# Kernel optimization log

Hardware: AMD Instinct MI355X
Metric: run time of the kernel (lower is better)

The kernel has to match this reference:

```python
import jax, jax.numpy as jnp
import numpy as np


def setup_inputs() -> dict:
    key = jax.random.key(0)
    k1, k2, k3, k4, k5 = jax.random.split(key, 5)
    B, H, W, C = 4, 64, 64, 512
    ratio = 8
    d = C // ratio  # 64
    x = jax.random.normal(k1, (B, H, W, C), dtype=jnp.float32)
    # 1x1 conv weights (no bias) == channel-mixing matrices, he_normal-ish scale
    Wq = jax.random.normal(k2, (C, d), dtype=jnp.float32) * np.sqrt(2.0 / C)
    Wk = jax.random.normal(k3, (C, d), dtype=jnp.float32) * np.sqrt(2.0 / C)
    Wv = jax.random.normal(k4, (C, C), dtype=jnp.float32) * np.sqrt(2.0 / C)
    gamma = jax.random.normal(k5, (1,), dtype=jnp.float32)
    return {"x": x, "Wq": Wq, "Wk": Wk, "Wv": Wv, "gamma": gamma}


def reference(x, Wq, Wk, Wv, gamma):
    B, H, W, C = x.shape
    N = H * W
    # 1x1 convs (no bias) are per-pixel channel matmuls
    q = jnp.einsum('bhwc,cd->bhwd', x, Wq).reshape(B, N, -1)  # [B,N,d]
    k = jnp.einsum('bhwc,cd->bhwd', x, Wk).reshape(B, N, -1)  # [B,N,d]
    v = jnp.einsum('bhwc,cd->bhwd', x, Wv).reshape(B, N, C)   # [B,N,C]
    # energy[b,i,j] = key_i . query_j  (batch_dot(key, query^T))
    energy = jnp.einsum('bid,bjd->bij', k, q)                 # [B,N,N]
    attn = jax.nn.softmax(energy, axis=-1)
    out = jnp.einsum('bij,bjc->bic', attn, v)                 # [B,N,C]
    out = out.reshape(B, H, W, C)
    return gamma * out
```

## Files before the change

kernel.cpp:

```cpp
#include <hip/hip_runtime.h>
#include <hip/hip_bf16.h>

typedef unsigned short u16;
typedef unsigned int   u32;
typedef __attribute__((ext_vector_type(8))) short short8;
typedef __attribute__((ext_vector_type(4))) float f32x4;
typedef __attribute__((ext_vector_type(4))) u16   u16x4;

#define MFMA16(a,b,c) __builtin_amdgcn_mfma_f32_16x16x32_bf16((a),(b),(c),0,0,0)

#define BATCH 4
#define NPIX  4096
#define CCH   512
#define DDIM  64
#define MFIX  64.0f

static __device__ __forceinline__ u16 f2bf(float f){
  __hip_bfloat16 h = __float2bfloat16(f);
  return __builtin_bit_cast(u16, h);
}
static __device__ __forceinline__ float bf2f(u16 u){
  __hip_bfloat16 h = __builtin_bit_cast(__hip_bfloat16, u);
  return __bfloat162float(h);
}

__global__ __launch_bounds__(256) void k_wconv(const f32x4* __restrict__ wv,
                                               u16x4* __restrict__ wvb){
  const int i = blockIdx.x*256 + threadIdx.x;
  #pragma unroll
  for (int it=0; it<4; ++it){
    int idx = i + it*16384;
    f32x4 v = wv[idx];
    u16x4 o;
    o[0]=f2bf(v[0]); o[1]=f2bf(v[1]); o[2]=f2bf(v[2]); o[3]=f2bf(v[3]);
    wvb[idx] = o;
  }
}

__global__ __launch_bounds__(256) void k_qkproj(const float* __restrict__ x,
                                                const float* __restrict__ Wq,
                                                const float* __restrict__ Wk,
                                                u16* __restrict__ qhi, u16* __restrict__ qlo,
                                                u16* __restrict__ khi, u16* __restrict__ klo,
                                                u16* __restrict__ xhi){
  __shared__ float xs[32][512];
  const int pix0 = blockIdx.x * 32;
  {
    const f32x4* xg = (const f32x4*)(x + (size_t)pix0*CCH);
    f32x4* xsv = (f32x4*)(&xs[0][0]);
    #pragma unroll
    for (int it=0; it<16; ++it) xsv[threadIdx.x + it*256] = xg[threadIdx.x + it*256];
  }
  __syncthreads();
  #pragma unroll
  for (int e=0; e<16; ++e){
    int idx4 = e*256 + threadIdx.x;
    int f = idx4*4;
    int row = f >> 9, col = f & 511;
    f32x4 v = *(const f32x4*)(&xs[row][col]);
    u16x4 o;
    o[0]=f2bf(v[0]); o[1]=f2bf(v[1]); o[2]=f2bf(v[2]); o[3]=f2bf(v[3]);
    *(u16x4*)(&xhi[(size_t)(pix0+row)*CCH + col]) = o;
  }
  const int col = threadIdx.x & 127;
  const int grp = threadIdx.x >> 7;
  const float* W = (col < 64) ? Wq : Wk;
  const int wc = col & 63;
  float acc[16];
  #pragma unroll
  for (int p=0;p<16;++p) acc[p] = 0.f;
  #pragma unroll 2
  for (int c=0;c<512;c+=4){
    float w0 = W[(c+0)*64 + wc];
    float w1 = W[(c+1)*64 + wc];
    float w2 = W[(c+2)*64 + wc];
    float w3 = W[(c+3)*64 + wc];
    #pragma unroll
    for (int p=0;p<16;++p){
      f32x4 xv = *(const f32x4*)(&xs[grp*16+p][c]);
      acc[p] += xv[0]*w0 + xv[1]*w1 + xv[2]*w2 + xv[3]*w3;
    }
  }
  #pragma unroll
  for (int p=0;p<16;++p){
    int pix = pix0 + grp*16 + p;
    float v = acc[p];
    u16 hi = f2bf(v);
    u16 lo = f2bf(v - bf2f(hi));
    if (col < 64){ qhi[pix*64+wc] = hi; qlo[pix*64+wc] = lo; }
    else         { khi[pix*64+wc] = hi; klo[pix*64+wc] = lo; }
  }
}

__global__ __launch_bounds__(256) void k_vproj(const u16* __restrict__ xhi,
                                               const u16* __restrict__ wvb,
                                               u16* __restrict__ vJB){
  __shared__ u16 As[64][72];
  __shared__ u16 Bs[64][266];
  const int pix0 = blockIdx.x * 64;
  const int c0   = blockIdx.y * 256;
  const int tid = threadIdx.x;
  const int w = tid >> 6, l = tid & 63;
  const int lg = l >> 4, ll = l & 15;
  f32x4 acc[4][4];
  #pragma unroll
  for (int mf=0;mf<4;++mf)
    #pragma unroll
    for (int nf=0;nf<4;++nf){ f32x4 z = {0.f,0.f,0.f,0.f}; acc[mf][nf] = z; }

  for (int ks=0; ks<8; ++ks){
    __syncthreads();
    #pragma unroll
    for (int it=0; it<2; ++it){
      int ch = tid + it*256; int r = ch>>3, c8 = ch&7;
      *(uint4*)(&As[r][c8*8]) = *(const uint4*)(&xhi[(size_t)(pix0+r)*CCH + ks*64 + c8*8]);
    }
    #pragma unroll
    for (int it=0; it<8; ++it){
      int ch = tid + it*256; int r = ch>>5, c32 = ch&31;
      uint4 d = *(const uint4*)(&wvb[(size_t)(ks*64+r)*CCH + c0 + c32*8]);
      u32* dst = (u32*)(&Bs[r][c32*8]);
      dst[0]=d.x; dst[1]=d.y; dst[2]=d.z; dst[3]=d.w;
    }
    __syncthreads();
    #pragma unroll
    for (int kc=0;kc<2;++kc){
      short8 a[4];
      #pragma unroll
      for (int mf=0;mf<4;++mf) a[mf] = *(const short8*)(&As[mf*16 + ll][kc*32 + lg*8]);
      #pragma unroll
      for (int nf=0;nf<4;++nf){
        short8 bb;
        int cc = w*64 + nf*16 + ll;
        #pragma unroll
        for (int e=0;e<8;++e) bb[e] = (short)Bs[kc*32 + lg*8 + e][cc];
        #pragma unroll
        for (int mf=0;mf<4;++mf) acc[mf][nf] = MFMA16(a[mf], bb, acc[mf][nf]);
      }
    }
  }
  #pragma unroll
  for (int mf=0;mf<4;++mf){
    #pragma unroll
    for (int nf=0;nf<4;++nf){
      int pix = pix0 + mf*16 + lg*4;
      int c   = c0 + w*64 + nf*16 + ll;
      int bb  = pix >> 12;
      int j   = pix & 4095;
      u16x4 o;
      #pragma unroll
      for (int r=0;r<4;++r) o[r] = f2bf(acc[mf][nf][r]);
      size_t off = (((size_t)bb*64 + (j>>6))*CCH + c)*64 + (j&63);
      *(u16x4*)(vJB + off) = o;
    }
  }
}

__global__ __launch_bounds__(512,4)
void k_attn(const u16* __restrict__ qhi, const u16* __restrict__ qlo,
            const u16* __restrict__ khi, const u16* __restrict__ klo,
            const u16* __restrict__ vJB, const float* __restrict__ gamma_p,
            float* __restrict__ out){
  __shared__ u16 Ps[2][64][72];
  __shared__ u16 Qs[2][64][72];
  __shared__ float l_s[64];
  const int bid = blockIdx.x;
  const int x  = bid & 7;
  const int b  = x >> 1, ch = x & 1;
  const int i0 = (bid >> 3) * 64;
  const int tid = threadIdx.x;
  const int w = tid >> 6, l = tid & 63;
  const int lg = l >> 4, ll = l & 15;
  const int iw = (w & 3) * 16;
  const int jw = (w >> 2) * 32;
  const int cw = ch*256 + w*32;

  const u16* qh_b  = qhi + (size_t)b*NPIX*DDIM;
  const u16* ql_b  = qlo + (size_t)b*NPIX*DDIM;
  const u16* vbase = vJB + (size_t)b*64*CCH*64;

  short8 kfh[2], kfl[2];
  #pragma unroll
  for (int kc=0;kc<2;++kc){
    size_t a = ((size_t)(b*NPIX + i0 + iw + ll))*DDIM + kc*32 + lg*8;
    kfh[kc] = *(const short8*)(khi + a);
    kfl[kc] = *(const short8*)(klo + a);
  }
  short8 ones;
  #pragma unroll
  for (int e=0;e<8;++e) ones[e] = (short)0x3F80;

  f32x4 acc[4][2];
  #pragma unroll
  for (int mf=0;mf<4;++mf)
    #pragma unroll
    for (int nf=0;nf<2;++nf){ f32x4 z = {0.f,0.f,0.f,0.f}; acc[mf][nf] = z; }
  f32x4 accl[4];
  #pragma unroll
  for (int mf=0;mf<4;++mf){ f32x4 z = {0.f,0.f,0.f,0.f}; accl[mf] = z; }

  const int sc0   = tid*2;
  const int spart = sc0 >> 9;
  const int srow  = (sc0 >> 3) & 63;
  const int sq    = sc0 & 7;
  const u16* sgl  = spart ? ql_b : qh_b;
  uint4 qr0, qr1;

  auto stage_load = [&](int j0){
    const u16* p = sgl + (size_t)(j0 + srow)*DDIM + sq*8;
    qr0 = *(const uint4*)p;
    qr1 = *(const uint4*)(p + 8);
  };
  auto stage_write = [&](){
    u16* d = &Qs[spart][srow][sq*8];
    *(uint4*)d       = qr0;
    *(uint4*)(d + 8) = qr1;
  };

  auto s_step = [&](int buf){
    #pragma unroll
    for (int jf=0;jf<2;++jf){
      f32x4 s = {0.f,0.f,0.f,0.f};
      #pragma unroll
      for (int kc=0;kc<2;++kc){
        short8 qh = *(const short8*)(&Qs[0][jw + jf*16 + ll][kc*32 + lg*8]);
        short8 ql = *(const short8*)(&Qs[1][jw + jf*16 + ll][kc*32 + lg*8]);
        s = MFMA16(qh, kfh[kc], s);
        s = MFMA16(ql, kfh[kc], s);
        s = MFMA16(qh, kfl[kc], s);
      }
      u16x4 pk;
      #pragma unroll
      for (int r=0;r<4;++r) pk[r] = f2bf(__expf(s[r] - MFIX));
      *(u16x4*)(&Ps[buf][iw + ll][jw + jf*16 + lg*4]) = pk;
    }
  };

  stage_load(0);
  stage_write();
  stage_load(64);
  __syncthreads();
  s_step(0);

  for (int t=0; t<64; ++t){
    const u16* vt = vbase + (size_t)t*CCH*64;
    short8 vb[4];
    #pragma unroll
    for (int kc=0;kc<2;++kc)
      #pragma unroll
      for (int nf=0;nf<2;++nf)
        vb[kc*2+nf] = *(const short8*)(vt + (size_t)(cw + nf*16 + ll)*64 + kc*32 + lg*8);

    __syncthreads();
    if (t < 63){
      stage_write();
      if (t < 62) stage_load(t*64 + 128);
    }
    __syncthreads();
    if (t < 63) s_step((t+1)&1);

    #pragma unroll
    for (int kc=0;kc<2;++kc){
      short8 pa[4];
      #pragma unroll
      for (int mf=0;mf<4;++mf) pa[mf] = *(const short8*)(&Ps[t&1][mf*16 + ll][kc*32 + lg*8]);
      #pragma unroll
      for (int nf=0;nf<2;++nf)
        #pragma unroll
        for (int mf=0;mf<4;++mf) acc[mf][nf] = MFMA16(pa[mf], vb[kc*2+nf], acc[mf][nf]);
      if (w == 0){
        #pragma unroll
        for (int mf=0;mf<4;++mf) accl[mf] = MFMA16(pa[mf], ones, accl[mf]);
      }
    }
  }

  if (w == 0 && ll == 0){
    #pragma unroll
    for (int mf=0;mf<4;++mf)
      #pragma unroll
      for (int r=0;r<4;++r) l_s[mf*16 + lg*4 + r] = accl[mf][r];
  }
  __syncthreads();
  const float gm = gamma_p[0];
  #pragma unroll
  for (int mf=0;mf<4;++mf){
    f32x4 inv;
    #pragma unroll
    for (int r=0;r<4;++r) inv[r] = gm / l_s[mf*16 + lg*4 + r];
    #pragma unroll
    for (int nf=0;nf<2;++nf)
      #pragma unroll
      for (int r=0;r<4;++r){
        int row = i0 + mf*16 + lg*4 + r;
        int c   = cw + nf*16 + ll;
        out[((size_t)(b*NPIX + row))*CCH + c] = acc[mf][nf][r] * inv[r];
      }
  }
}

extern "C" void kernel_launch(void* const* d_in, const int* in_sizes, int n_in,
                              void* d_out, int out_size, void* d_ws, size_t ws_size,
                              hipStream_t stream) {
  (void)in_sizes; (void)n_in; (void)out_size; (void)ws_size;
  const float* x  = (const float*)d_in[0];
  const float* Wq = (const float*)d_in[1];
  const float* Wk = (const float*)d_in[2];
  const float* Wv = (const float*)d_in[3];
  const float* gm = (const float*)d_in[4];
  float* out = (float*)d_out;

  u16* qhi = (u16*)d_ws;
  u16* qlo = qhi + (size_t)BATCH*NPIX*DDIM;
  u16* khi = qlo + (size_t)BATCH*NPIX*DDIM;
  u16* klo = khi + (size_t)BATCH*NPIX*DDIM;
  u16* vJB = klo + (size_t)BATCH*NPIX*DDIM;

  u16* xhi = (u16*)d_out;
  u16* wvb = xhi + (size_t)BATCH*NPIX*CCH;

  k_qkproj<<<dim3(512), dim3(256), 0, stream>>>(x, Wq, Wk, qhi, qlo, khi, klo, xhi);
  k_wconv<<<dim3(64), dim3(256), 0, stream>>>((const f32x4*)Wv, (u16x4*)wvb);
  k_vproj<<<dim3(256,2), dim3(256), 0, stream>>>(xhi, wvb, vJB);
  k_attn<<<dim3(512), dim3(512), 0, stream>>>(qhi, qlo, khi, klo, vJB, gm, out);
}
```

Measured before the change: 224.5 us.

## Double-buffer Q tiles to drop a barrier and sum softmax denominators in registers

Q staging in shared memory is now double-buffered and prefetched two tiles ahead, so each iteration of the main loop needs one barrier instead of two. The softmax row sum is accumulated in fp32 from the exp values inside s_step. It is then reduced with lane shuffles and shared memory, replacing the extra MFMA-with-ones work that only wave 0 did and that unbalanced the waves. The cost is more shared memory for Q and a row sum taken from fp32 values rather than the rounded bf16 ones, which shifts numerics slightly.

```diff
diff --git a/kernel.cpp b/kernel.cpp
--- a/kernel.cpp
+++ b/kernel.cpp
@@ -161,8 +161,9 @@
             const u16* __restrict__ khi, const u16* __restrict__ klo,
             const u16* __restrict__ vJB, const float* __restrict__ gamma_p,
             float* __restrict__ out){
+  __shared__ u16 Qs[2][2][64][72];
   __shared__ u16 Ps[2][64][72];
-  __shared__ u16 Qs[2][64][72];
+  __shared__ float l_half[8][16];
   __shared__ float l_s[64];
   const int bid = blockIdx.x;
   const int x  = bid & 7;
@@ -186,18 +187,13 @@
     kfh[kc] = *(const short8*)(khi + a);
     kfl[kc] = *(const short8*)(klo + a);
   }
-  short8 ones;
-  #pragma unroll
-  for (int e=0;e<8;++e) ones[e] = (short)0x3F80;
 
   f32x4 acc[4][2];
   #pragma unroll
   for (int mf=0;mf<4;++mf)
     #pragma unroll
     for (int nf=0;nf<2;++nf){ f32x4 z = {0.f,0.f,0.f,0.f}; acc[mf][nf] = z; }
-  f32x4 accl[4];
-  #pragma unroll
-  for (int mf=0;mf<4;++mf){ f32x4 z = {0.f,0.f,0.f,0.f}; accl[mf] = z; }
+  float lsum = 0.f;
 
   const int sc0   = tid*2;
   const int spart = sc0 >> 9;
@@ -211,34 +207,39 @@
     qr0 = *(const uint4*)p;
     qr1 = *(const uint4*)(p + 8);
   };
-  auto stage_write = [&](){
-    u16* d = &Qs[spart][srow][sq*8];
+  auto stage_write = [&](int buf){
+    u16* d = &Qs[buf][spart][srow][sq*8];
     *(uint4*)d       = qr0;
     *(uint4*)(d + 8) = qr1;
   };
 
-  auto s_step = [&](int buf){
+  auto s_step = [&](int u){
+    const int buf = u & 1;
     #pragma unroll
     for (int jf=0;jf<2;++jf){
       f32x4 s = {0.f,0.f,0.f,0.f};
       #pragma unroll
       for (int kc=0;kc<2;++kc){
-        short8 qh = *(const short8*)(&Qs[0][jw + jf*16 + ll][kc*32 + lg*8]);
-        short8 ql = *(const short8*)(&Qs[1][jw + jf*16 + ll][kc*32 + lg*8]);
+        short8 qh = *(const short8*)(&Qs[buf][0][jw + jf*16 + ll][kc*32 + lg*8]);
+        short8 ql = *(const short8*)(&Qs[buf][1][jw + jf*16 + ll][kc*32 + lg*8]);
         s = MFMA16(qh, kfh[kc], s);
         s = MFMA16(ql, kfh[kc], s);
         s = MFMA16(qh, kfl[kc], s);
       }
       u16x4 pk;
       #pragma unroll
-      for (int r=0;r<4;++r) pk[r] = f2bf(__expf(s[r] - MFIX));
+      for (int r=0;r<4;++r){
+        float p = __expf(s[r] - MFIX);
+        lsum += p;
+        pk[r] = f2bf(p);
+      }
       *(u16x4*)(&Ps[buf][iw + ll][jw + jf*16 + lg*4]) = pk;
     }
   };
 
-  stage_load(0);
-  stage_write();
-  stage_load(64);
+  stage_load(0);    stage_write(0);
+  stage_load(64);   stage_write(1);
+  stage_load(128);
   __syncthreads();
   s_step(0);
 
@@ -252,12 +253,9 @@
         vb[kc*2+nf] = *(const short8*)(vt + (size_t)(cw + nf*16 + ll)*64 + kc*32 + lg*8);
 
     __syncthreads();
-    if (t < 63){
-      stage_write();
-      if (t < 62) stage_load(t*64 + 128);
-    }
-    __syncthreads();
-    if (t < 63) s_step((t+1)&1);
+    if (t < 62) stage_write(t & 1);
+    if (t < 61) stage_load((t+3) * 64);
+    if (t < 63) s_step(t + 1);
 
     #pragma unroll
     for (int kc=0;kc<2;++kc){
@@ -268,20 +266,16 @@
       for (int nf=0;nf<2;++nf)
         #pragma unroll
         for (int mf=0;mf<4;++mf) acc[mf][nf] = MFMA16(pa[mf], vb[kc*2+nf], acc[mf][nf]);
-      if (w == 0){
-        #pragma unroll
-        for (int mf=0;mf<4;++mf) accl[mf] = MFMA16(pa[mf], ones, accl[mf]);
-      }
-    }
-  }
-
-  if (w == 0 && ll == 0){
-    #pragma unroll
-    for (int mf=0;mf<4;++mf)
-      #pragma unroll
-      for (int r=0;r<4;++r) l_s[mf*16 + lg*4 + r] = accl[mf][r];
-  }
+    }
+  }
+
+  lsum += __shfl_xor(lsum, 16);
+  lsum += __shfl_xor(lsum, 32);
+  if (lg == 0) l_half[w][ll] = lsum;
   __syncthreads();
+  if (w < 4 && lg == 0) l_s[iw + ll] = l_half[w][ll] + l_half[w + 4][ll];
+  __syncthreads();
+
   const float gm = gamma_p[0];
   #pragma unroll
   for (int mf=0;mf<4;++mf){
```

Result: no change. 227.0 us (+1.1%).
